# Optimization experiments

Hardware: AMD Instinct MI355X
Metric: run time of the kernel (lower is better)

Reference implementation:

```python
import math
import jax, jax.numpy as jnp
import numpy as np

SQRT_2_OVER_PI = 0.7978845608028654
EPS = 1e-5
EPS_VAR = 1e-4
NORM_EPS = 1e-12  # F.normalize default eps


def _gelu_tanh(x):
    return 0.5 * x * (1.0 + jnp.tanh(SQRT_2_OVER_PI * (x + 0.044715 * x ** 3)))


def _normalize(v, axis):
    n = jnp.linalg.norm(v, axis=axis, keepdims=True)
    return v / jnp.maximum(n, NORM_EPS)


def setup_inputs() -> dict:
    key = jax.random.key(0)
    k_x, k_m, k_o = jax.random.split(key, 3)
    B, T, D = 8, 2048, 512
    x = jax.random.normal(k_x, (B, T, D), dtype=jnp.float32)
    ema_mean = 0.1 * jax.random.normal(k_m, (D,), dtype=jnp.float32)
    ema_sq = ema_mean ** 2 + 1.0  # ensures positive variance, like a warmed-up EMA
    ema_out = jax.random.normal(k_o, (D,), dtype=jnp.float32)
    f32 = lambda v: jnp.asarray(v, dtype=jnp.float32)
    return {
        "x": x,
        "ema_mean": ema_mean,
        "ema_sq": ema_sq,
        "ema_out": ema_out,
        "log_tau": f32(math.log(2.0)),
        "log_beta_up": f32(math.log(math.exp(0.5) - 1.0)),
        "log_beta_dn": f32(math.log(math.exp(0.5) - 1.0)),
        "log_gamma": f32(math.log(math.exp(1.0) - 1.0)),
        "log_sigma_nn": f32(math.log(math.exp(1.0) - 1.0)),
        "log_w_nn": f32(math.log(math.exp(1.0) - 1.0)),
    }


def reference(x, ema_mean, ema_sq, ema_out, log_tau, log_beta_up,
              log_beta_dn, log_gamma, log_sigma_nn, log_w_nn):
    # Steady-state (_ready=True) forward path.
    sg = jax.lax.stop_gradient
    sp = jax.nn.softplus
    tau = jnp.exp(log_tau)
    beta_up, beta_dn = sp(log_beta_up), sp(log_beta_dn)
    gamma, sigma_nn, w_nn = sp(log_gamma), sp(log_sigma_nn), sp(log_w_nn)

    out = _gelu_tanh(x)  # [B,T,D]

    # --- per-channel asymmetric EMA z-score gate (z detached) ---
    var = jnp.clip(ema_sq - ema_mean ** 2, EPS_VAR, None)  # [D]
    std = jnp.sqrt(var)
    z = sg((x - ema_mean) / (std + EPS))  # [B,T,D]
    up_arm = beta_up * jax.nn.relu(jnp.tanh(gamma * z))
    dn_arm = beta_dn * jax.nn.relu(jnp.tanh(-gamma * z))
    gate_hist = jnp.clip(1.0 + up_arm - dn_arm, 0.05, 8.0)

    # --- within-sequence nearest-neighbor novelty gate (sim detached) ---
    T = x.shape[1]
    x_n = _normalize(sg(x), axis=-1)  # [B,T,D]
    sim = jnp.einsum('btd,bsd->bts', x_n, x_n)  # [B,T,T]
    sim = jnp.where(jnp.eye(T, dtype=bool)[None], -2.0, sim)
    nn_sim = jnp.max(sim, axis=-1)  # [B,T]
    novelty_nn = (1.0 - nn_sim) * 0.5
    surp_nn = sg(jnp.tanh(sigma_nn * novelty_nn))  # sigma_nn under no_grad
    gate_nn = (1.0 + w_nn * surp_nn)[..., None]  # [B,T,1]

    # --- cosine-to-EMA-output gate (fully detached, incl. tau) ---
    out_n = _normalize(out, axis=-1)
    ema_n = _normalize(ema_out, axis=0)  # [D]
    cos_sim = jnp.clip(jnp.sum(out_n * ema_n, axis=-1), -1.0, 1.0)  # [B,T]
    gate_cos = sg(jnp.exp(-tau * cos_sim))[..., None]  # [B,T,1]

    return out * gate_hist * gate_nn * gate_cos
```

## Files before the change

### kernel.cpp

```cpp
#include <hip/hip_runtime.h>
#include <hip/hip_bf16.h>
#include <math.h>

#define BB 8
#define TT 2048
#define DD 512
#define NSL 32

typedef __attribute__((ext_vector_type(8))) short bf16x8;
typedef __attribute__((ext_vector_type(4))) float f32x4;
typedef __attribute__((ext_vector_type(4))) int i32x4;

__device__ inline float softplus_f(float v) { return log1pf(expf(v)); }

__device__ inline float tanh_fast(float y) {
    float e = __builtin_amdgcn_exp2f(y * 2.8853900817779268f);
    return 1.0f - 2.0f * __builtin_amdgcn_rcpf(e + 1.0f);
}
__device__ inline float exp_fast(float y) {
    return __builtin_amdgcn_exp2f(y * 1.4426950408889634f);
}

__device__ inline unsigned short cvt_bf16(float f) {
    __hip_bfloat16 h = (__hip_bfloat16)f;
    return *reinterpret_cast<unsigned short*>(&h);
}
__device__ inline float bf2f(unsigned short h) {
    unsigned int u = ((unsigned int)h) << 16;
    return __uint_as_float(u);
}

__device__ inline void load_lds16(const void* g, void* l) {
    __builtin_amdgcn_global_load_lds(
        (const __attribute__((address_space(1))) unsigned int*)g,
        (__attribute__((address_space(3))) unsigned int*)l, 16, 0, 0);
}

__global__ __launch_bounds__(256) void k1_elem(
    const float* __restrict__ x, const float* __restrict__ ema_mean,
    const float* __restrict__ ema_sq, const float* __restrict__ ema_out,
    const float* __restrict__ p_log_tau, const float* __restrict__ p_lbu,
    const float* __restrict__ p_lbd, const float* __restrict__ p_lg,
    unsigned char* __restrict__ xn8, unsigned short* __restrict__ po) {
    const int row = blockIdx.x * 4 + (threadIdx.x >> 6);
    const int lane = threadIdx.x & 63;
    const size_t base = (size_t)row * DD;
    const int j0 = lane * 4, j1 = 256 + lane * 4;

    float4 xx0 = *reinterpret_cast<const float4*>(x + base + j0);
    float4 xx1 = *reinterpret_cast<const float4*>(x + base + j1);
    float4 mm0 = *reinterpret_cast<const float4*>(ema_mean + j0);
    float4 mm1 = *reinterpret_cast<const float4*>(ema_mean + j1);
    float4 qq0 = *reinterpret_cast<const float4*>(ema_sq + j0);
    float4 qq1 = *reinterpret_cast<const float4*>(ema_sq + j1);
    float4 eo0 = *reinterpret_cast<const float4*>(ema_out + j0);
    float4 eo1 = *reinterpret_cast<const float4*>(ema_out + j1);

    const float tau = expf(p_log_tau[0]);
    const float beta_up = softplus_f(p_lbu[0]);
    const float beta_dn = softplus_f(p_lbd[0]);
    const float gamma = softplus_f(p_lg[0]);

    float xv[8], pg[8];
    float sx2 = 0.f, so2 = 0.f, sod = 0.f, se2 = 0.f;
    float vv[8] = {xx0.x, xx0.y, xx0.z, xx0.w, xx1.x, xx1.y, xx1.z, xx1.w};
    float vm[8] = {mm0.x, mm0.y, mm0.z, mm0.w, mm1.x, mm1.y, mm1.z, mm1.w};
    float vq[8] = {qq0.x, qq0.y, qq0.z, qq0.w, qq1.x, qq1.y, qq1.z, qq1.w};
    float ve[8] = {eo0.x, eo0.y, eo0.z, eo0.w, eo1.x, eo1.y, eo1.z, eo1.w};
#pragma unroll
    for (int e = 0; e < 8; ++e) {
        float xf = vv[e];
        xv[e] = xf;
        float x3 = xf * xf * xf;
        float gl = 0.5f * xf * (1.0f + tanh_fast(0.7978845608028654f * (xf + 0.044715f * x3)));
        float var = fmaxf(vq[e] - vm[e] * vm[e], 1e-4f);
        float istd = __builtin_amdgcn_rcpf(sqrtf(var) + 1e-5f);
        float z = (xf - vm[e]) * istd;
        float th = tanh_fast(gamma * z);
        float up = beta_up * fmaxf(th, 0.0f);
        float dn = beta_dn * fmaxf(-th, 0.0f);
        float gh = fminf(fmaxf(1.0f + up - dn, 0.05f), 8.0f);
        pg[e] = gl * gh;
        sx2 += xf * xf;
        so2 += gl * gl;
        sod += gl * ve[e];
        se2 += ve[e] * ve[e];
    }
#pragma unroll
    for (int off = 32; off; off >>= 1) {
        sx2 += __shfl_xor(sx2, off);
        so2 += __shfl_xor(so2, off);
        sod += __shfl_xor(sod, off);
        se2 += __shfl_xor(se2, off);
    }
    const float qscale = 127.0f * __builtin_amdgcn_rcpf(fmaxf(sqrtf(sx2), 1e-12f));
    const float inv_en = __builtin_amdgcn_rcpf(fmaxf(sqrtf(se2), 1e-12f));
    float cosv = sod * inv_en * __builtin_amdgcn_rcpf(fmaxf(sqrtf(so2), 1e-12f));
    cosv = fminf(fmaxf(cosv, -1.0f), 1.0f);
    const float gcos = exp_fast(-tau * cosv);

#pragma unroll
    for (int c = 0; c < 2; ++c) {
        const int j = c * 256 + lane * 4;
        ushort4 pb;
        pb.x = cvt_bf16(pg[c * 4 + 0] * gcos);
        pb.y = cvt_bf16(pg[c * 4 + 1] * gcos);
        pb.z = cvt_bf16(pg[c * 4 + 2] * gcos);
        pb.w = cvt_bf16(pg[c * 4 + 3] * gcos);
        *reinterpret_cast<ushort4*>(po + base + j) = pb;
        int q0 = __float2int_rn(xv[c * 4 + 0] * qscale);
        int q1 = __float2int_rn(xv[c * 4 + 1] * qscale);
        int q2 = __float2int_rn(xv[c * 4 + 2] * qscale);
        int q3 = __float2int_rn(xv[c * 4 + 3] * qscale);
        int pk = (q0 & 255) | ((q1 & 255) << 8) | ((q2 & 255) << 16) | (q3 << 24);
        *reinterpret_cast<int*>(xn8 + base + j) = pk;
    }
}

__global__ __launch_bounds__(256, 3) void k2_nn(const unsigned char* __restrict__ xn8,
                                                float* __restrict__ partial) {
    __shared__ char lds[49152];

    const int tid = threadIdx.x;
    const int wave = tid >> 6;
    const int lane = tid & 63;
    const int r15 = lane & 15;
    const int kgrp = lane >> 4;
    const int wr = wave >> 1;
    const int wc = wave & 1;

    const int bid = blockIdx.x;
    const int b = bid & 7;
    int t = bid >> 3;
    int tm = 0;
    while (t >= 16 - tm) { t -= 16 - tm; ++tm; }
    const int tn = tm + t;

    const size_t bbase = (size_t)b * TT * DD;
    const unsigned char* Ag = xn8 + bbase + (size_t)tm * 128 * DD;
    const unsigned char* Bg = xn8 + bbase + (size_t)tn * 128 * DD;

    i32x4 acc[4][4];
#pragma unroll
    for (int i = 0; i < 4; ++i)
#pragma unroll
        for (int j = 0; j < 4; ++j) acc[i][j] = (i32x4){0, 0, 0, 0};

    auto stage = [&](int slot, int kt) {
#pragma unroll
        for (int l = 0; l < 2; ++l) {
            const int o = l * 4096 + tid * 16;
            const int sup = o >> 7;
            const int w = (o & 127) ^ ((sup & 7) << 4);
            const int row = sup * 2 + (w >> 6);
            const int cb = w & 63;
            load_lds16(Ag + (size_t)row * DD + kt * 64 + cb, lds + slot * 16384 + o);
            load_lds16(Bg + (size_t)row * DD + kt * 64 + cb, lds + slot * 16384 + 8192 + o);
        }
    };

#define LADDR(R) \
    (((R) >> 1) * 128 + (((((R) & 1) << 6) + (kgrp << 4)) ^ ((((R) >> 1) & 7) << 4)))

    auto compute = [&](int slot) {
        const char* sA = lds + slot * 16384;
        const char* sB = sA + 8192;
        i32x4 av[4], bv[4];
#pragma unroll
        for (int ni = 0; ni < 4; ++ni)
            bv[ni] = *(const i32x4*)(sB + LADDR(wc * 64 + ni * 16 + r15));
#pragma unroll
        for (int mi = 0; mi < 4; ++mi)
            av[mi] = *(const i32x4*)(sA + LADDR(wr * 64 + mi * 16 + r15));
        __builtin_amdgcn_s_setprio(1);
#pragma unroll
        for (int mi = 0; mi < 4; ++mi)
#pragma unroll
            for (int ni = 0; ni < 4; ++ni)
                acc[mi][ni] = __builtin_amdgcn_mfma_i32_16x16x64_i8(av[mi], bv[ni],
                                                                    acc[mi][ni], 0, 0, 0);
        __builtin_amdgcn_s_setprio(0);
    };
#undef LADDR

    stage(0, 0);
    stage(1, 1);
    asm volatile("s_waitcnt vmcnt(4)" ::: "memory");
    __builtin_amdgcn_s_barrier();
    __builtin_amdgcn_sched_barrier(0);

#pragma unroll
    for (int kt = 0; kt < 8; ++kt) {
        if (kt + 2 < 8) stage((kt + 2) % 3, kt + 2);
        compute(kt % 3);
        if (kt < 7) {
            if (kt + 2 < 8)
                asm volatile("s_waitcnt vmcnt(4)" ::: "memory");
            else
                asm volatile("s_waitcnt vmcnt(0)" ::: "memory");
            __builtin_amdgcn_s_barrier();
            __builtin_amdgcn_sched_barrier(0);
        }
    }

    const float inv_qq = 1.0f / (127.0f * 127.0f);
    const bool diag = (tm == tn);
    float accf[4][4][4];
#pragma unroll
    for (int mi = 0; mi < 4; ++mi)
#pragma unroll
        for (int ni = 0; ni < 4; ++ni)
#pragma unroll
            for (int rr = 0; rr < 4; ++rr) {
                float e = (float)acc[mi][ni][rr] * inv_qq;
                if (diag) {
                    const int rl = wr * 64 + mi * 16 + kgrp * 4 + rr;
                    const int cl = wc * 64 + ni * 16 + r15;
                    if (rl == cl) e = -2.0f;
                }
                accf[mi][ni][rr] = e;
            }
    float rmx[4][4];
#pragma unroll
    for (int mi = 0; mi < 4; ++mi)
#pragma unroll
        for (int rr = 0; rr < 4; ++rr) {
            float v = fmaxf(fmaxf(accf[mi][0][rr], accf[mi][1][rr]),
                            fmaxf(accf[mi][2][rr], accf[mi][3][rr]));
            v = fmaxf(v, __shfl_xor(v, 1));
            v = fmaxf(v, __shfl_xor(v, 2));
            v = fmaxf(v, __shfl_xor(v, 4));
            v = fmaxf(v, __shfl_xor(v, 8));
            rmx[mi][rr] = v;
        }
    float cmx[4];
#pragma unroll
    for (int ni = 0; ni < 4; ++ni) {
        float v = -2.0f;
#pragma unroll
        for (int mi = 0; mi < 4; ++mi)
#pragma unroll
            for (int rr = 0; rr < 4; ++rr) v = fmaxf(v, accf[mi][ni][rr]);
        v = fmaxf(v, __shfl_xor(v, 16));
        v = fmaxf(v, __shfl_xor(v, 32));
        cmx[ni] = v;
    }
    __syncthreads();
    float* rbuf = (float*)lds;
    float* cbuf = (float*)(lds + 1024);
    if (r15 == 0) {
#pragma unroll
        for (int mi = 0; mi < 4; ++mi)
#pragma unroll
            for (int rr = 0; rr < 4; ++rr)
                rbuf[(wr * 64 + mi * 16 + kgrp * 4 + rr) * 2 + wc] = rmx[mi][rr];
    }
    if (kgrp == 0) {
#pragma unroll
        for (int ni = 0; ni < 4; ++ni)
            cbuf[(wc * 64 + ni * 16 + r15) * 2 + wr] = cmx[ni];
    }
    __syncthreads();
    if (tid < 128) {
        const float v = fmaxf(rbuf[tid * 2 + 0], rbuf[tid * 2 + 1]);
        partial[((size_t)b * TT + tm * 128 + tid) * NSL + tn] = v;
    } else if (!diag) {
        const int c = tid - 128;
        const float v = fmaxf(cbuf[c * 2 + 0], cbuf[c * 2 + 1]);
        partial[((size_t)b * TT + tn * 128 + c) * NSL + 16 + tm] = v;
    }
}

__global__ __launch_bounds__(256) void k3_scale(float* __restrict__ out,
                                                const unsigned short* __restrict__ po,
                                                const float* __restrict__ partial,
                                                const float* __restrict__ p_lsn,
                                                const float* __restrict__ p_lwn) {
    const int row = blockIdx.x * 4 + (threadIdx.x >> 6);
    const int lane = threadIdx.x & 63;
    const float sigma_nn = softplus_f(p_lsn[0]);
    const float w_nn = softplus_f(p_lwn[0]);

    const int p = (row & (TT - 1)) >> 7;
    float v = -2.0f;
    if (lane < 16) {
        if (lane >= p) v = partial[(size_t)row * NSL + lane];
    } else if (lane < NSL) {
        if (lane - 16 < p) v = partial[(size_t)row * NSL + lane];
    }
    v = fmaxf(v, __shfl_xor(v, 1));
    v = fmaxf(v, __shfl_xor(v, 2));
    v = fmaxf(v, __shfl_xor(v, 4));
    v = fmaxf(v, __shfl_xor(v, 8));
    v = fmaxf(v, __shfl_xor(v, 16));
    v = fmaxf(v, __shfl_xor(v, 32));
    const float g = 1.0f + w_nn * tanh_fast(sigma_nn * 0.5f * (1.0f - v));

    const size_t base = (size_t)row * DD + lane * 8;
    ushort4 p0 = *reinterpret_cast<const ushort4*>(po + base);
    ushort4 p1 = *reinterpret_cast<const ushort4*>(po + base + 4);
    float4 o0, o1;
    o0.x = bf2f(p0.x) * g; o0.y = bf2f(p0.y) * g;
    o0.z = bf2f(p0.z) * g; o0.w = bf2f(p0.w) * g;
    o1.x = bf2f(p1.x) * g; o1.y = bf2f(p1.y) * g;
    o1.z = bf2f(p1.z) * g; o1.w = bf2f(p1.w) * g;
    *reinterpret_cast<float4*>(out + base) = o0;
    *reinterpret_cast<float4*>(out + base + 4) = o1;
}

extern "C" void kernel_launch(void* const* d_in, const int* in_sizes, int n_in,
                              void* d_out, int out_size, void* d_ws, size_t ws_size,
                              hipStream_t stream) {
    const float* x = (const float*)d_in[0];
    const float* ema_mean = (const float*)d_in[1];
    const float* ema_sq = (const float*)d_in[2];
    const float* ema_out = (const float*)d_in[3];
    const float* log_tau = (const float*)d_in[4];
    const float* log_beta_up = (const float*)d_in[5];
    const float* log_beta_dn = (const float*)d_in[6];
    const float* log_gamma = (const float*)d_in[7];
    const float* log_sigma_nn = (const float*)d_in[8];
    const float* log_w_nn = (const float*)d_in[9];

    char* ws = (char*)d_ws;
    unsigned char* XN8 = (unsigned char*)ws;
    unsigned short* PO = (unsigned short*)(ws + 8388608);
    float* partial = (float*)(ws + 8388608 + 16777216);
    float* out = (float*)d_out;

    hipLaunchKernelGGL(k1_elem, dim3(BB * TT / 4), dim3(256), 0, stream, x, ema_mean, ema_sq,
                       ema_out, log_tau, log_beta_up, log_beta_dn, log_gamma, XN8, PO);
    hipLaunchKernelGGL(k2_nn, dim3(BB * 136), dim3(256), 0, stream, XN8, partial);
    hipLaunchKernelGGL(k3_scale, dim3(BB * TT / 4), dim3(256), 0, stream, out, PO, partial,
                       log_sigma_nn, log_w_nn);
}
```

Baseline: 60.01 us.

## Load int8 MFMA operands directly from global memory instead of LDS staging

The NN-similarity kernel no longer uses a triple-buffered LDS pipeline with global_load_lds and barriers. Each wave now reads its A/B fragments straight from global memory (relying on L1/L2 for reuse across waves), and launch bounds rise to 4 blocks per SM since LDS use drops to two small reduction buffers. This removes the LDS traffic and barrier synchronisation but duplicates global loads across waves and loses explicit prefetch overlap, so the MFMAs may stall on memory latency.

```diff
diff --git a/kernel.cpp b/kernel.cpp
--- a/kernel.cpp
+++ b/kernel.cpp
@@ -28,12 +28,6 @@
 __device__ inline float bf2f(unsigned short h) {
     unsigned int u = ((unsigned int)h) << 16;
     return __uint_as_float(u);
-}
-
-__device__ inline void load_lds16(const void* g, void* l) {
-    __builtin_amdgcn_global_load_lds(
-        (const __attribute__((address_space(1))) unsigned int*)g,
-        (__attribute__((address_space(3))) unsigned int*)l, 16, 0, 0);
 }
 
 __global__ __launch_bounds__(256) void k1_elem(
@@ -117,9 +111,10 @@
     }
 }
 
-__global__ __launch_bounds__(256, 3) void k2_nn(const unsigned char* __restrict__ xn8,
+__global__ __launch_bounds__(256, 4) void k2_nn(const unsigned char* __restrict__ xn8,
                                                 float* __restrict__ partial) {
-    __shared__ char lds[49152];
+    __shared__ float rbuf[128 * 2];
+    __shared__ float cbuf[128 * 2];
 
     const int tid = threadIdx.x;
     const int wave = tid >> 6;
@@ -140,67 +135,34 @@
     const unsigned char* Ag = xn8 + bbase + (size_t)tm * 128 * DD;
     const unsigned char* Bg = xn8 + bbase + (size_t)tn * 128 * DD;
 
+    const i32x4* pA[4];
+    const i32x4* pB[4];
+#pragma unroll
+    for (int mi = 0; mi < 4; ++mi)
+        pA[mi] = (const i32x4*)(Ag + (size_t)(wr * 64 + mi * 16 + r15) * DD + kgrp * 16);
+#pragma unroll
+    for (int ni = 0; ni < 4; ++ni)
+        pB[ni] = (const i32x4*)(Bg + (size_t)(wc * 64 + ni * 16 + r15) * DD + kgrp * 16);
+
     i32x4 acc[4][4];
 #pragma unroll
     for (int i = 0; i < 4; ++i)
 #pragma unroll
         for (int j = 0; j < 4; ++j) acc[i][j] = (i32x4){0, 0, 0, 0};
 
-    auto stage = [&](int slot, int kt) {
-#pragma unroll
-        for (int l = 0; l < 2; ++l) {
-            const int o = l * 4096 + tid * 16;
-            const int sup = o >> 7;
-            const int w = (o & 127) ^ ((sup & 7) << 4);
-            const int row = sup * 2 + (w >> 6);
-            const int cb = w & 63;
-            load_lds16(Ag + (size_t)row * DD + kt * 64 + cb, lds + slot * 16384 + o);
-            load_lds16(Bg + (size_t)row * DD + kt * 64 + cb, lds + slot * 16384 + 8192 + o);
-        }
-    };
-
-#define LADDR(R) \
-    (((R) >> 1) * 128 + (((((R) & 1) << 6) + (kgrp << 4)) ^ ((((R) >> 1) & 7) << 4)))
-
-    auto compute = [&](int slot) {
-        const char* sA = lds + slot * 16384;
-        const char* sB = sA + 8192;
+#pragma unroll
+    for (int kt = 0; kt < 8; ++kt) {
         i32x4 av[4], bv[4];
 #pragma unroll
-        for (int ni = 0; ni < 4; ++ni)
-            bv[ni] = *(const i32x4*)(sB + LADDR(wc * 64 + ni * 16 + r15));
-#pragma unroll
-        for (int mi = 0; mi < 4; ++mi)
-            av[mi] = *(const i32x4*)(sA + LADDR(wr * 64 + mi * 16 + r15));
-        __builtin_amdgcn_s_setprio(1);
+        for (int ni = 0; ni < 4; ++ni) bv[ni] = pB[ni][kt * 4];
+#pragma unroll
+        for (int mi = 0; mi < 4; ++mi) av[mi] = pA[mi][kt * 4];
 #pragma unroll
         for (int mi = 0; mi < 4; ++mi)
 #pragma unroll
             for (int ni = 0; ni < 4; ++ni)
                 acc[mi][ni] = __builtin_amdgcn_mfma_i32_16x16x64_i8(av[mi], bv[ni],
                                                                     acc[mi][ni], 0, 0, 0);
-        __builtin_amdgcn_s_setprio(0);
-    };
-#undef LADDR
-
-    stage(0, 0);
-    stage(1, 1);
-    asm volatile("s_waitcnt vmcnt(4)" ::: "memory");
-    __builtin_amdgcn_s_barrier();
-    __builtin_amdgcn_sched_barrier(0);
-
-#pragma unroll
-    for (int kt = 0; kt < 8; ++kt) {
-        if (kt + 2 < 8) stage((kt + 2) % 3, kt + 2);
-        compute(kt % 3);
-        if (kt < 7) {
-            if (kt + 2 < 8)
-                asm volatile("s_waitcnt vmcnt(4)" ::: "memory");
-            else
-                asm volatile("s_waitcnt vmcnt(0)" ::: "memory");
-            __builtin_amdgcn_s_barrier();
-            __builtin_amdgcn_sched_barrier(0);
-        }
     }
 
     const float inv_qq = 1.0f / (127.0f * 127.0f);
@@ -245,9 +207,6 @@
         v = fmaxf(v, __shfl_xor(v, 32));
         cmx[ni] = v;
     }
-    __syncthreads();
-    float* rbuf = (float*)lds;
-    float* cbuf = (float*)(lds + 1024);
     if (r15 == 0) {
 #pragma unroll
         for (int mi = 0; mi < 4; ++mi)
```

Measured after the change: 84.02 us. 1.4x slower.
